# Kernel tuning notes

Hardware: AMD Instinct MI355X
Metric: run time of the kernel (lower is better)

The kernel has to match this reference:

```python
import jax, jax.numpy as jnp
import numpy as np

B, E = 256, 65536          # batch, embed_dim
S = 256                    # seq_len = sqrt(E)
D = E // S                 # per-token input dim = 256
HID = 512                  # hidden_dim
HD = HID // 2              # per-direction GRU hidden = 256
GH = 128                   # gcn_hidden_dim
K = 5                      # k_neighbors


def setup_inputs() -> dict:
    key = jax.random.key(0)
    ks = jax.random.split(key, 16)
    s = 0.02
    return {
        "C_masked": jax.random.normal(ks[0], (B, E), jnp.float32),
        "W_proj": jax.random.normal(ks[1], (HID, D), jnp.float32) * s,
        "b_proj": jnp.zeros((HID,), jnp.float32),
        "Wih_f": jax.random.normal(ks[2], (3 * HD, HID), jnp.float32) * s,
        "Whh_f": jax.random.normal(ks[3], (3 * HD, HD), jnp.float32) * s,
        "bih_f": jnp.zeros((3 * HD,), jnp.float32),
        "bhh_f": jnp.zeros((3 * HD,), jnp.float32),
        "Wih_b": jax.random.normal(ks[4], (3 * HD, HID), jnp.float32) * s,
        "Whh_b": jax.random.normal(ks[5], (3 * HD, HD), jnp.float32) * s,
        "bih_b": jnp.zeros((3 * HD,), jnp.float32),
        "bhh_b": jnp.zeros((3 * HD,), jnp.float32),
        "W_gcn1": jax.random.normal(ks[6], (HID, GH), jnp.float32) * 0.01,
        "W_gcn2": jax.random.normal(ks[7], (GH, HID), jnp.float32) * 0.01,
    }


def _gru_dir(x, Wih, Whh, bih, bhh, reverse):
    # x: (B, S, IN) -> (B, S, HD). PyTorch GRU cell equations.
    gi = jnp.einsum('bsd,hd->bsh', x, Wih) + bih          # (B,S,3HD)
    gi = jnp.swapaxes(gi, 0, 1)                            # (S,B,3HD)
    h0 = jnp.zeros((x.shape[0], HD), x.dtype)

    def step(h, gi_t):
        gh = h @ Whh.T + bhh
        i_r, i_z, i_n = jnp.split(gi_t, 3, axis=-1)
        h_r, h_z, h_n = jnp.split(gh, 3, axis=-1)
        r = jax.nn.sigmoid(i_r + h_r)
        z = jax.nn.sigmoid(i_z + h_z)
        n = jnp.tanh(i_n + r * h_n)
        h_new = (1.0 - z) * n + z * h
        return h_new, h_new

    _, ys = jax.lax.scan(step, h0, gi, reverse=reverse)    # (S,B,HD), index-aligned
    return jnp.swapaxes(ys, 0, 1)


def reference(C_masked, W_proj, b_proj,
              Wih_f, Whh_f, bih_f, bhh_f,
              Wih_b, Whh_b, bih_b, bhh_b,
              W_gcn1, W_gcn2):
    b, e = C_masked.shape
    s = int(np.sqrt(e))
    d = e // s
    C_seq = C_masked.reshape(b, s, d)
    C_proj = jnp.einsum('bsd,hd->bsh', C_seq, W_proj) + b_proj   # (B,S,HID)

    # BiGRU (eval mode; dropout inactive)
    h_f = _gru_dir(C_proj, Wih_f, Whh_f, bih_f, bhh_f, reverse=False)
    h_b = _gru_dir(C_proj, Wih_b, Whh_b, bih_b, bhh_b, reverse=True)
    H = jnp.concatenate([h_f, h_b], axis=-1)                     # (B,S,HID)

    # KNN graph: cosine sim -> topk -> scatter 1.0 -> add self loops
    Hn = H / jnp.maximum(jnp.linalg.norm(H, axis=-1, keepdims=True), 1e-12)
    sim = jnp.einsum('bnd,bmd->bnm', Hn, Hn)                     # (B,S,S)
    topk_idx = jax.lax.top_k(sim, K)[1]                          # (B,S,K)
    bi = jnp.arange(b)[:, None, None]
    ni = jnp.arange(s)[None, :, None]
    A = jnp.zeros((b, s, s), H.dtype).at[bi, ni, topk_idx].set(1.0)
    A = A + jnp.eye(s, dtype=H.dtype)[None]

    # D^{-1/2} A D^{-1/2}
    deg = A.sum(axis=-1) + 1e-8
    dinv = deg ** -0.5
    A_norm = dinv[:, :, None] * A * dinv[:, None, :]

    # 2-layer GCN (dropout inactive in eval)
    Z1 = jax.nn.relu(jnp.einsum('bnm,bmh->bnh', A_norm, H @ W_gcn1))
    Z = jnp.einsum('bnm,bmh->bnh', A_norm, Z1 @ W_gcn2)
    return Z
```

## Files before the change

kernel.cpp:

```cpp
#include <hip/hip_runtime.h>
#include <hip/hip_fp16.h>
#include <cstdint>
#include <cmath>

typedef _Float16 f16x8 __attribute__((ext_vector_type(8)));
typedef float f32x4 __attribute__((ext_vector_type(4)));

#define MFMA16(A, B, C) __builtin_amdgcn_mfma_f32_16x16x32_f16(A, B, C, 0, 0, 0)
#define LO_SCALE 2048.0f
#define LO_INV   4.8828125e-4f

#define GBM 128
#define GBN 128
#define GBK 16

template<bool TRANSB>
__global__ __launch_bounds__(256)
void gemm_f32(int M, int N, int K,
              const float* __restrict__ A, long long sA,
              const float* __restrict__ B, long long sB,
              float* __restrict__ Cc, long long sC,
              const float* __restrict__ bias,
              const float* __restrict__ rsA,
              const float* __restrict__ rsB)
{
    const int z = blockIdx.z;
    A  += (size_t)z * (size_t)sA;
    B  += (size_t)z * (size_t)sB;
    Cc += (size_t)z * (size_t)sC;

    const int bm = blockIdx.y * GBM;
    const int bn = blockIdx.x * GBN;
    const int tid = threadIdx.x;
    const int tx = tid & 15;
    const int ty = tid >> 4;

    __shared__ float As[GBK][GBM + 4];
    __shared__ float Bs[GBK][GBN + 4];

    float acc[8][8];
#pragma unroll
    for (int i = 0; i < 8; ++i)
#pragma unroll
        for (int j = 0; j < 8; ++j) acc[i][j] = 0.0f;

    const int lr = tid >> 2;
    const int lk = (tid & 3) << 2;
    const int kb_n = tid >> 5;
    const int nb_n = (tid & 31) << 2;

    float sa0 = 1.f, sa1 = 1.f, sb0 = 1.f, sb1 = 1.f;
    if (rsA) {
        sa0 = rsA[(size_t)z * M + bm + lr];
        sa1 = rsA[(size_t)z * M + bm + lr + 64];
    }
    if (TRANSB && rsB) {
        sb0 = rsB[(size_t)z * N + bn + lr];
        sb1 = rsB[(size_t)z * N + bn + lr + 64];
    }

    float4 pa0, pa1, pb0, pb1;

    auto gload = [&](int kt) {
        const float* pA = A + (size_t)(bm + lr) * K + kt * GBK + lk;
        pa0 = *(const float4*)pA;
        pa1 = *(const float4*)(pA + (size_t)64 * K);
        if (TRANSB) {
            const float* pB = B + (size_t)(bn + lr) * K + kt * GBK + lk;
            pb0 = *(const float4*)pB;
            pb1 = *(const float4*)(pB + (size_t)64 * K);
        } else {
            const float* pB = B + (size_t)(kt * GBK + kb_n) * N + bn + nb_n;
            pb0 = *(const float4*)pB;
            pb1 = *(const float4*)(pB + (size_t)8 * N);
        }
    };
    auto sstore = [&]() {
        As[lk + 0][lr] = pa0.x * sa0; As[lk + 1][lr] = pa0.y * sa0;
        As[lk + 2][lr] = pa0.z * sa0; As[lk + 3][lr] = pa0.w * sa0;
        As[lk + 0][lr + 64] = pa1.x * sa1; As[lk + 1][lr + 64] = pa1.y * sa1;
        As[lk + 2][lr + 64] = pa1.z * sa1; As[lk + 3][lr + 64] = pa1.w * sa1;
        if (TRANSB) {
            Bs[lk + 0][lr] = pb0.x * sb0; Bs[lk + 1][lr] = pb0.y * sb0;
            Bs[lk + 2][lr] = pb0.z * sb0; Bs[lk + 3][lr] = pb0.w * sb0;
            Bs[lk + 0][lr + 64] = pb1.x * sb1; Bs[lk + 1][lr + 64] = pb1.y * sb1;
            Bs[lk + 2][lr + 64] = pb1.z * sb1; Bs[lk + 3][lr + 64] = pb1.w * sb1;
        } else {
            *(float4*)&Bs[kb_n][nb_n]     = pb0;
            *(float4*)&Bs[kb_n + 8][nb_n] = pb1;
        }
    };

    const int nkt = K / GBK;
    gload(0);
    sstore();
    __syncthreads();
    for (int kt = 0; kt < nkt; ++kt) {
        if (kt + 1 < nkt) gload(kt + 1);
#pragma unroll
        for (int k = 0; k < GBK; ++k) {
            float4 a0 = *(const float4*)&As[k][ty * 8];
            float4 a1 = *(const float4*)&As[k][ty * 8 + 4];
            float4 b0 = *(const float4*)&Bs[k][tx * 8];
            float4 b1 = *(const float4*)&Bs[k][tx * 8 + 4];
            float av[8] = {a0.x, a0.y, a0.z, a0.w, a1.x, a1.y, a1.z, a1.w};
            float bv[8] = {b0.x, b0.y, b0.z, b0.w, b1.x, b1.y, b1.z, b1.w};
#pragma unroll
            for (int i = 0; i < 8; ++i)
#pragma unroll
                for (int j = 0; j < 8; ++j)
                    acc[i][j] = fmaf(av[i], bv[j], acc[i][j]);
        }
        __syncthreads();
        if (kt + 1 < nkt) { sstore(); __syncthreads(); }
    }

    float bb[8];
#pragma unroll
    for (int j = 0; j < 8; ++j) bb[j] = bias ? bias[bn + tx * 8 + j] : 0.0f;
#pragma unroll
    for (int i = 0; i < 8; ++i) {
        const int row = bm + ty * 8 + i;
        float* cp = Cc + (size_t)row * N + bn + tx * 8;
        float4 o0 = make_float4(acc[i][0] + bb[0], acc[i][1] + bb[1],
                                acc[i][2] + bb[2], acc[i][3] + bb[3]);
        float4 o1 = make_float4(acc[i][4] + bb[4], acc[i][5] + bb[5],
                                acc[i][6] + bb[6], acc[i][7] + bb[7]);
        *(float4*)cp = o0;
        *(float4*)(cp + 4) = o1;
    }
}

__global__ void bias_combine(const float* __restrict__ Wih, const float* __restrict__ b_proj,
                             const float* __restrict__ bih, float* __restrict__ bcomb)
{
    const int j = blockIdx.x * blockDim.x + threadIdx.x;
    if (j >= 768) return;
    float s = bih[j];
    for (int k = 0; k < 512; ++k) s = fmaf(Wih[(size_t)j * 512 + k], b_proj[k], s);
    bcomb[j] = s;
}

__global__ __launch_bounds__(256)
void pack_w(const float* __restrict__ W, unsigned short* __restrict__ pack)
{
    const int idx = blockIdx.x * 256 + threadIdx.x;
    if (idx >= 768 * 256) return;
    const int n = idx >> 8;
    const int k = idx & 255;
    const float w = W[idx];
    const __half hi = __float2half(w);
    const __half lo = __float2half((w - __half2float(hi)) * LO_SCALE);
    const int nt = n >> 4;
    const int lane = ((k >> 3) & 3) * 16 + (n & 15);
    const int j = k & 7;
    const int kc = k >> 5;
    const size_t base = ((size_t)(nt * 8 + kc) * 2) * 512 + lane * 8 + j;
    pack[base]       = __half_as_ushort(hi);
    pack[base + 512] = __half_as_ushort(lo);
}

__global__ __launch_bounds__(256)
void pack_bk(const float* __restrict__ W, unsigned short* __restrict__ pack,
             int K, int N)
{
    const int idx = blockIdx.x * 256 + threadIdx.x;
    if (idx >= K * N) return;
    const int k = idx / N;
    const int n = idx - k * N;
    const float w = W[idx];
    const __half hi = __float2half(w);
    const __half lo = __float2half((w - __half2float(hi)) * LO_SCALE);
    const int nt = n >> 4;
    const int kc = k >> 5;
    const int lane = ((k >> 3) & 3) * 16 + (n & 15);
    const int j = k & 7;
    const int KC = K >> 5;
    const size_t base = ((size_t)(nt * KC + kc) * 2) * 512 + lane * 8 + j;
    pack[base]       = __half_as_ushort(hi);
    pack[base + 512] = __half_as_ushort(lo);
}

__global__ __launch_bounds__(512)
void gi_gemm_c(const float* __restrict__ Cm, const unsigned short* __restrict__ pack,
               const float* __restrict__ bcomb, float* __restrict__ gi, int t0)
{
    const int tid = threadIdx.x;
    const int w = tid >> 6, l = tid & 63;
    const int l15 = l & 15, l4 = l >> 4;
    const int bgrp = blockIdx.x >> 1;
    const int half = blockIdx.x & 1;
    const size_t m0 = (size_t)bgrp * 256 + t0 + half * 64;
    const size_t o0 = (size_t)bgrp * 128 + half * 64;

    __shared__ unsigned short alds[2][64 * 256];

    {
        const int row = tid >> 3;
        const int seg = (tid & 7) * 32;
        const float4* src = (const float4*)(Cm + (m0 + row) * 256 + seg);
        const int sw = (row & 7) << 3;
#pragma unroll
        for (int i = 0; i < 8; ++i) {
            float4 v = src[i];
            float vv[4] = {v.x, v.y, v.z, v.w};
#pragma unroll
            for (int e = 0; e < 4; ++e) {
                const float x = vv[e];
                const __half hi = __float2half(x);
                const __half lo = __float2half((x - __half2float(hi)) * LO_SCALE);
                const int ad = (row << 8) + ((seg + i * 4 + e) ^ sw);
                alds[0][ad] = __half_as_ushort(hi);
                alds[1][ad] = __half_as_ushort(lo);
            }
        }
    }
    __syncthreads();

    const int mt = w >> 1, nh = w & 1;
    f32x4 acc[24];
#pragma unroll
    for (int i = 0; i < 24; ++i) acc[i] = (f32x4){0.f, 0.f, 0.f, 0.f};

    const int ar = mt * 16 + l15;
    const int arow = ar << 8;
    const int asw = (ar & 7) << 3;

#pragma unroll
    for (int kc = 0; kc < 8; ++kc) {
        const int ad = arow + ((kc * 32 + l4 * 8) ^ asw);
        const f16x8 ahi = *(const f16x8*)&alds[0][ad];
        const f16x8 alo = *(const f16x8*)&alds[1][ad];
#pragma unroll
        for (int nt = 0; nt < 24; ++nt) {
            const int nt_lin = nh * 24 + nt;
            const uint4* bp = (const uint4*)(pack + ((size_t)(nt_lin * 8 + kc) * 2) * 512);
            uint4 bh4 = bp[l];
            uint4 bl4 = bp[64 + l];
            const f16x8 Bhi = *reinterpret_cast<const f16x8*>(&bh4);
            const f16x8 Blo = *reinterpret_cast<const f16x8*>(&bl4);
            acc[nt] = MFMA16(ahi, Bhi, acc[nt]);
            f32x4 t2 = (f32x4){0.f, 0.f, 0.f, 0.f};
            t2 = MFMA16(ahi, Blo, t2);
            t2 = MFMA16(alo, Bhi, t2);
#pragma unroll
            for (int r = 0; r < 4; ++r) acc[nt][r] = fmaf(LO_INV, t2[r], acc[nt][r]);
        }
    }

#pragma unroll
    for (int nt = 0; nt < 24; ++nt) {
        const int n = (nh * 24 + nt) * 16 + l15;
        const float bb = bcomb[n];
#pragma unroll
        for (int r = 0; r < 4; ++r) {
            const size_t om = o0 + mt * 16 + l4 * 4 + r;
            __builtin_nontemporal_store(acc[nt][r] + bb, &gi[om * 768 + n]);
        }
    }
}

__global__ __launch_bounds__(1024)
void gru_scan_v9(const float* __restrict__ gi_fc, const float* __restrict__ gi_bc,
                 const float* __restrict__ Whh_f, const float* __restrict__ Whh_b,
                 const float* __restrict__ bhh_f, const float* __restrict__ bhh_b,
                 float* __restrict__ H, float* __restrict__ hstate, int phase)
{
    const int bid = blockIdx.x;
    const int xcd = bid & 7;
    const int dir = xcd >> 2;
    const int grp = (bid >> 3) * 4 + (xcd & 3);
    const float* __restrict__ gi  = dir ? gi_bc : gi_fc;
    const float* __restrict__ Whh = dir ? Whh_b : Whh_f;
    const float* __restrict__ bhh = dir ? bhh_b : bhh_f;
    const int b0 = grp * 8;
    const int t0 = dir ? (128 - phase * 128) : (phase * 128);

    const int tid = threadIdx.x;
    const int j = tid >> 2;
    const int q = tid & 3;
    const int bA = q, bB = q + 4;

    __shared__ float hb[2][8][256];

    float hregA, hregB;
    if (phase == 0) { hregA = 0.f; hregB = 0.f; }
    else {
        hregA = hstate[((size_t)dir * 256 + b0 + bA) * 256 + j];
        hregB = hstate[((size_t)dir * 256 + b0 + bB) * 256 + j];
    }
    hb[0][bA][j] = hregA;
    hb[0][bB][j] = hregB;

    const float bh_r = bhh[j], bh_z = bhh[j + 256], bh_n = bhh[j + 512];
    const float* __restrict__ Wr = Whh + (size_t)j * 256 + q * 4;
    const float* __restrict__ Wz = Whh + (size_t)(j + 256) * 256 + q * 4;
    const float* __restrict__ Wn = Whh + (size_t)(j + 512) * 256 + q * 4;

    __syncthreads();

    int p = 0;
    for (int tau = 0; tau < 128; ++tau) {
        const int sc = dir ? (127 - tau) : tau;
        const int tt = t0 + sc;

        const float* gpA = gi + ((size_t)(b0 + bA) * 128 + sc) * 768 + j;
        const float* gpB = gi + ((size_t)(b0 + bB) * 128 + sc) * 768 + j;
        const float grA = __builtin_nontemporal_load(gpA);
        const float gzA = __builtin_nontemporal_load(gpA + 256);
        const float gnA = __builtin_nontemporal_load(gpA + 512);
        const float grB = __builtin_nontemporal_load(gpB);
        const float gzB = __builtin_nontemporal_load(gpB + 256);
        const float gnB = __builtin_nontemporal_load(gpB + 512);

        float ar[8], az[8], an[8];
#pragma unroll
        for (int b = 0; b < 8; ++b) { ar[b] = 0.f; az[b] = 0.f; an[b] = 0.f; }

        float4 wrP[3], wzP[3], wnP[3];
#pragma unroll
        for (int i = 0; i < 3; ++i) {
            wrP[i] = *(const float4*)(Wr + i * 16);
            wzP[i] = *(const float4*)(Wz + i * 16);
            wnP[i] = *(const float4*)(Wn + i * 16);
        }

#pragma unroll
        for (int u = 0; u < 16; ++u) {
            const int s3 = u % 3;
            const float4 wr = wrP[s3], wz = wzP[s3], wn = wnP[s3];
            if (u + 3 < 16) {
                wrP[s3] = *(const float4*)(Wr + (u + 3) * 16);
                wzP[s3] = *(const float4*)(Wz + (u + 3) * 16);
                wnP[s3] = *(const float4*)(Wn + (u + 3) * 16);
            }
            const int ha = u * 16 + q * 4;
#pragma unroll
            for (int b = 0; b < 8; ++b) {
                const float4 hv = *(const float4*)&hb[p][b][ha];
                ar[b] = fmaf(wr.x, hv.x, ar[b]); ar[b] = fmaf(wr.y, hv.y, ar[b]);
                ar[b] = fmaf(wr.z, hv.z, ar[b]); ar[b] = fmaf(wr.w, hv.w, ar[b]);
                az[b] = fmaf(wz.x, hv.x, az[b]); az[b] = fmaf(wz.y, hv.y, az[b]);
                az[b] = fmaf(wz.z, hv.z, az[b]); az[b] = fmaf(wz.w, hv.w, az[b]);
                an[b] = fmaf(wn.x, hv.x, an[b]); an[b] = fmaf(wn.y, hv.y, an[b]);
                an[b] = fmaf(wn.z, hv.z, an[b]); an[b] = fmaf(wn.w, hv.w, an[b]);
            }
        }

#pragma unroll
        for (int b = 0; b < 8; ++b) {
            ar[b] += __shfl_xor(ar[b], 1); ar[b] += __shfl_xor(ar[b], 2);
            az[b] += __shfl_xor(az[b], 1); az[b] += __shfl_xor(az[b], 2);
            an[b] += __shfl_xor(an[b], 1); an[b] += __shfl_xor(an[b], 2);
        }

        const float prA = (q == 0) ? ar[0] : (q == 1) ? ar[1] : (q == 2) ? ar[2] : ar[3];
        const float pzA = (q == 0) ? az[0] : (q == 1) ? az[1] : (q == 2) ? az[2] : az[3];
        const float pnA = (q == 0) ? an[0] : (q == 1) ? an[1] : (q == 2) ? an[2] : an[3];
        const float prB = (q == 0) ? ar[4] : (q == 1) ? ar[5] : (q == 2) ? ar[6] : ar[7];
        const float pzB = (q == 0) ? az[4] : (q == 1) ? az[5] : (q == 2) ? az[6] : az[7];
        const float pnB = (q == 0) ? an[4] : (q == 1) ? an[5] : (q == 2) ? an[6] : an[7];

        float rr = 1.0f / (1.0f + expf(-(grA + prA + bh_r)));
        float zz = 1.0f / (1.0f + expf(-(gzA + pzA + bh_z)));
        float nn = tanhf(gnA + rr * (pnA + bh_n));
        hregA = (1.0f - zz) * nn + zz * hregA;
        rr = 1.0f / (1.0f + expf(-(grB + prB + bh_r)));
        zz = 1.0f / (1.0f + expf(-(gzB + pzB + bh_z)));
        nn = tanhf(gnB + rr * (pnB + bh_n));
        hregB = (1.0f - zz) * nn + zz * hregB;

        hb[p ^ 1][bA][j] = hregA;
        hb[p ^ 1][bB][j] = hregB;
        __builtin_nontemporal_store(
            hregA, &H[((size_t)(b0 + bA) * 256 + tt) * 512 + dir * 256 + j]);
        __builtin_nontemporal_store(
            hregB, &H[((size_t)(b0 + bB) * 256 + tt) * 512 + dir * 256 + j]);
        __syncthreads();
        p ^= 1;
    }

    hstate[((size_t)dir * 256 + b0 + bA) * 256 + j] = hregA;
    hstate[((size_t)dir * 256 + b0 + bB) * 256 + j] = hregB;
}

__global__ __launch_bounds__(256)
void rownorm(const float* __restrict__ H, float* __restrict__ rinv)
{
    const int row  = blockIdx.x * 4 + (threadIdx.x >> 6);
    const int lane = threadIdx.x & 63;
    const float4* p = (const float4*)(H + (size_t)row * 512);
    float ss = 0.f;
    float4 v = p[lane];
    ss += v.x * v.x + v.y * v.y + v.z * v.z + v.w * v.w;
    v = p[lane + 64];
    ss += v.x * v.x + v.y * v.y + v.z * v.z + v.w * v.w;
#pragma unroll
    for (int off = 32; off >= 1; off >>= 1) ss += __shfl_xor(ss, off);
    if (lane == 0) rinv[row] = 1.0f / fmaxf(sqrtf(ss), 1e-12f);
}

__global__ __launch_bounds__(512)
void sim_mfma(const float* __restrict__ H, const float* __restrict__ rinv,
              float* __restrict__ sim)
{
    const int b = blockIdx.x;
    const int tid = threadIdx.x;
    const int w = tid >> 6, l = tid & 63;
    const int l15 = l & 15, l4 = l >> 4;

    __shared__ unsigned short st[2][256][40];

    f32x4 acc[2][16];
#pragma unroll
    for (int m = 0; m < 2; ++m)
#pragma unroll
        for (int n = 0; n < 16; ++n) acc[m][n] = (f32x4){0.f, 0.f, 0.f, 0.f};

    const int sr = tid >> 1;
    const int sh = (tid & 1) * 16;
    const float rv = rinv[b * 256 + sr];
    const float* hrow = H + ((size_t)b * 256 + sr) * 512;

    for (int kc = 0; kc < 16; ++kc) {
        if (kc) __syncthreads();
        {
            const float4* src = (const float4*)(hrow + kc * 32 + sh);
#pragma unroll
            for (int i = 0; i < 4; ++i) {
                float4 v = src[i];
                float vv[4] = {v.x, v.y, v.z, v.w};
                ushort4 h4, l4v;
                unsigned short* hp = (unsigned short*)&h4;
                unsigned short* lp = (unsigned short*)&l4v;
#pragma unroll
                for (int e = 0; e < 4; ++e) {
                    const float x = vv[e] * rv;
                    const __half hi = __float2half(x);
                    const __half lo = __float2half((x - __half2float(hi)) * LO_SCALE);
                    hp[e] = __half_as_ushort(hi);
                    lp[e] = __half_as_ushort(lo);
                }
                *(ushort4*)&st[0][sr][sh + i * 4] = h4;
                *(ushort4*)&st[1][sr][sh + i * 4] = l4v;
            }
        }
        __syncthreads();

        f16x8 ahi[2], alo[2];
#pragma unroll
        for (int m = 0; m < 2; ++m) {
            const int row = (w * 2 + m) * 16 + l15;
            ahi[m] = *(const f16x8*)&st[0][row][l4 * 8];
            alo[m] = *(const f16x8*)&st[1][row][l4 * 8];
        }
#pragma unroll
        for (int nt = 0; nt < 16; ++nt) {
            const int col = nt * 16 + l15;
            const f16x8 bhi = *(const f16x8*)&st[0][col][l4 * 8];
            const f16x8 blo = *(const f16x8*)&st[1][col][l4 * 8];
#pragma unroll
            for (int m = 0; m < 2; ++m) {
                acc[m][nt] = MFMA16(ahi[m], bhi, acc[m][nt]);
                f32x4 t2 = (f32x4){0.f, 0.f, 0.f, 0.f};
                t2 = MFMA16(ahi[m], blo, t2);
                t2 = MFMA16(alo[m], bhi, t2);
#pragma unroll
                for (int r = 0; r < 4; ++r)
                    acc[m][nt][r] = fmaf(LO_INV, t2[r], acc[m][nt][r]);
            }
        }
    }

#pragma unroll
    for (int m = 0; m < 2; ++m) {
        const int row0 = (w * 2 + m) * 16 + l4 * 4;
#pragma unroll
        for (int nt = 0; nt < 16; ++nt)
#pragma unroll
            for (int r = 0; r < 4; ++r)
                sim[((size_t)b * 256 + row0 + r) * 256 + nt * 16 + l15] = acc[m][nt][r];
    }
}

template<int KDIM, int NDIM, int NT_PER>
__global__ __launch_bounds__(512)
void gcn_mm(const float* __restrict__ X, const unsigned short* __restrict__ pack,
            float* __restrict__ Y)
{
    const int tid = threadIdx.x;
    const int w = tid >> 6, l = tid & 63;
    const int l15 = l & 15, l4 = l >> 4;
    const int m0 = blockIdx.x * 64;
    constexpr int KC = KDIM / 32;

    __shared__ unsigned short a[2][64 * KDIM];

    {
        const int row = tid >> 3;
        const int seg = (tid & 7) * (KDIM / 8);
        const float4* src = (const float4*)(X + (size_t)(m0 + row) * KDIM + seg);
        const int sw = (row & 7) << 3;
#pragma unroll
        for (int i = 0; i < KDIM / 32; ++i) {
            float4 v = src[i];
            float vv[4] = {v.x, v.y, v.z, v.w};
#pragma unroll
            for (int e = 0; e < 4; ++e) {
                const float x = vv[e];
                const __half hi = __float2half(x);
                const __half lo = __float2half((x - __half2float(hi)) * LO_SCALE);
                const int ad = row * KDIM + ((seg + i * 4 + e) ^ sw);
                a[0][ad] = __half_as_ushort(hi);
                a[1][ad] = __half_as_ushort(lo);
            }
        }
    }
    __syncthreads();

    const int mt = w >> 1, nh = w & 1;
    f32x4 acc[NT_PER];
#pragma unroll
    for (int i = 0; i < NT_PER; ++i) acc[i] = (f32x4){0.f, 0.f, 0.f, 0.f};

    const int arow = mt * 16 + l15;
    const int abase = arow * KDIM;
    const int asw = (arow & 7) << 3;

#pragma unroll
    for (int kc = 0; kc < KC; ++kc) {
        const int ad = abase + ((kc * 32 + l4 * 8) ^ asw);
        const f16x8 ahi = *(const f16x8*)&a[0][ad];
        const f16x8 alo = *(const f16x8*)&a[1][ad];
#pragma unroll
        for (int ntl = 0; ntl < NT_PER; ++ntl) {
            const int nt = nh * NT_PER + ntl;
            const uint4* bp = (const uint4*)(pack + ((size_t)(nt * KC + kc) * 2) * 512);
            uint4 bh4 = bp[l];
            uint4 bl4 = bp[64 + l];
            const f16x8 Bhi = *reinterpret_cast<const f16x8*>(&bh4);
            const f16x8 Blo = *reinterpret_cast<const f16x8*>(&bl4);
            acc[ntl] = MFMA16(ahi, Bhi, acc[ntl]);
            f32x4 t2 = (f32x4){0.f, 0.f, 0.f, 0.f};
            t2 = MFMA16(ahi, Blo, t2);
            t2 = MFMA16(alo, Bhi, t2);
#pragma unroll
            for (int r = 0; r < 4; ++r) acc[ntl][r] = fmaf(LO_INV, t2[r], acc[ntl][r]);
        }
    }

#pragma unroll
    for (int ntl = 0; ntl < NT_PER; ++ntl) {
        const int n = (nh * NT_PER + ntl) * 16 + l15;
#pragma unroll
        for (int r = 0; r < 4; ++r) {
            const int m = m0 + mt * 16 + l4 * 4 + r;
            Y[(size_t)m * NDIM + n] = acc[ntl][r];
        }
    }
}

__global__ __launch_bounds__(256)
void topk5(const float* __restrict__ sim, int* __restrict__ idx)
{
    const int row = blockIdx.x * 256 + threadIdx.x;
    const float* p = sim + (size_t)row * 256;
    float bv0 = -1e30f, bv1 = -1e30f, bv2 = -1e30f, bv3 = -1e30f, bv4 = -1e30f;
    int   bi0 = 0, bi1 = 0, bi2 = 0, bi3 = 0, bi4 = 0;
    for (int m4 = 0; m4 < 64; ++m4) {
        float4 v4 = *(const float4*)(p + m4 * 4);
        float vv[4] = {v4.x, v4.y, v4.z, v4.w};
#pragma unroll
        for (int c = 0; c < 4; ++c) {
            float v = vv[c];
            int   m = m4 * 4 + c;
            if (v > bv0) {
                if (v > bv1) {
                    bv0 = bv1; bi0 = bi1;
                    if (v > bv2) {
                        bv1 = bv2; bi1 = bi2;
                        if (v > bv3) {
                            bv2 = bv3; bi2 = bi3;
                            if (v > bv4) { bv3 = bv4; bi3 = bi4; bv4 = v; bi4 = m; }
                            else         { bv3 = v;  bi3 = m; }
                        } else { bv2 = v; bi2 = m; }
                    } else { bv1 = v; bi1 = m; }
                } else { bv0 = v; bi0 = m; }
            }
        }
    }
    int* o = idx + (size_t)row * 5;
    o[0] = bi0; o[1] = bi1; o[2] = bi2; o[3] = bi3; o[4] = bi4;
}

template<bool RELU, int DIM>
__global__ __launch_bounds__(128)
void gcn_agg(const float* __restrict__ X, const int* __restrict__ idxs,
             float* __restrict__ outp, float cnorm)
{
    const int row = blockIdx.x;
    const int bbase = row & ~255;
    const int* id = idxs + (size_t)row * 5;
    const int i0 = bbase + id[0];
    const int i1 = bbase + id[1];
    const int i2 = bbase + id[2];
    const int i3 = bbase + id[3];
    const int i4 = bbase + id[4];
    const int t = threadIdx.x;
    if (DIM == 512) {
        const float4* Xp = (const float4*)X;
        float4 a = Xp[(size_t)row * 128 + t];
        float4 v;
        v = Xp[(size_t)i0 * 128 + t]; a.x += v.x; a.y += v.y; a.z += v.z; a.w += v.w;
        v = Xp[(size_t)i1 * 128 + t]; a.x += v.x; a.y += v.y; a.z += v.z; a.w += v.w;
        v = Xp[(size_t)i2 * 128 + t]; a.x += v.x; a.y += v.y; a.z += v.z; a.w += v.w;
        v = Xp[(size_t)i3 * 128 + t]; a.x += v.x; a.y += v.y; a.z += v.z; a.w += v.w;
        v = Xp[(size_t)i4 * 128 + t]; a.x += v.x; a.y += v.y; a.z += v.z; a.w += v.w;
        a.x *= cnorm; a.y *= cnorm; a.z *= cnorm; a.w *= cnorm;
        if (RELU) {
            a.x = fmaxf(a.x, 0.f); a.y = fmaxf(a.y, 0.f);
            a.z = fmaxf(a.z, 0.f); a.w = fmaxf(a.w, 0.f);
        }
        ((float4*)outp)[(size_t)row * 128 + t] = a;
    } else {
        float a = X[(size_t)row * 128 + t];
        a += X[(size_t)i0 * 128 + t];
        a += X[(size_t)i1 * 128 + t];
        a += X[(size_t)i2 * 128 + t];
        a += X[(size_t)i3 * 128 + t];
        a += X[(size_t)i4 * 128 + t];
        a *= cnorm;
        if (RELU) a = fmaxf(a, 0.f);
        outp[(size_t)row * 128 + t] = a;
    }
}

extern "C" void kernel_launch(void* const* d_in, const int* in_sizes, int n_in,
                              void* d_out, int out_size, void* d_ws, size_t ws_size,
                              hipStream_t stream)
{
    (void)in_sizes; (void)n_in; (void)out_size; (void)ws_size;

    const float* C_masked = (const float*)d_in[0];
    const float* W_proj   = (const float*)d_in[1];
    const float* b_proj   = (const float*)d_in[2];
    const float* Wih_f    = (const float*)d_in[3];
    const float* Whh_f    = (const float*)d_in[4];
    const float* bih_f    = (const float*)d_in[5];
    const float* bhh_f    = (const float*)d_in[6];
    const float* Wih_b    = (const float*)d_in[7];
    const float* Whh_b    = (const float*)d_in[8];
    const float* bih_b    = (const float*)d_in[9];
    const float* bhh_b    = (const float*)d_in[10];
    const float* W_gcn1   = (const float*)d_in[11];
    const float* W_gcn2   = (const float*)d_in[12];
    float* out = (float*)d_out;

    char* ws = (char*)d_ws;
    size_t o = 0;
    auto take = [&](size_t bytes) {
        size_t r = o;
        o = (o + bytes + 255) & ~(size_t)255;
        return r;
    };
    const size_t WCOMB_B = (size_t)768 * 256 * 4;
    const size_t PACK_B  = (size_t)48 * 8 * 2 * 512 * 2;
    const size_t PACKG_B = (size_t)262144;
    const size_t o_wcf  = take(WCOMB_B);
    const size_t o_wcb  = take(WCOMB_B);
    const size_t o_bcf  = take(768 * 4);
    const size_t o_bcb  = take(768 * 4);
    const size_t o_rinv = take((size_t)65536 * 4);
    const size_t o_topk = take((size_t)65536 * 5 * 4);
    const size_t o_pwf  = take(PACK_B);
    const size_t o_pwb  = take(PACK_B);
    const size_t o_pg1  = take(PACKG_B);
    const size_t o_pg2  = take(PACKG_B);
    const size_t o_hst  = take((size_t)512 * 256 * 4);
    const size_t regionA = o;

    const size_t GIC_BYTES = (size_t)256 * 128 * 768 * 4;

    float* wcomb_f = (float*)(ws + o_wcf);
    float* wcomb_b = (float*)(ws + o_wcb);
    float* bcomb_f = (float*)(ws + o_bcf);
    float* bcomb_b = (float*)(ws + o_bcb);
    float* rinv    = (float*)(ws + o_rinv);
    int*   topk    = (int*)(ws + o_topk);
    unsigned short* packWf = (unsigned short*)(ws + o_pwf);
    unsigned short* packWb = (unsigned short*)(ws + o_pwb);
    unsigned short* packG1 = (unsigned short*)(ws + o_pg1);
    unsigned short* packG2 = (unsigned short*)(ws + o_pg2);
    float* hstate = (float*)(ws + o_hst);

    float* gi_fc = (float*)(ws + regionA);
    float* gi_bc = (float*)(ws + regionA + GIC_BYTES);
    float* Hbuf  = (float*)(ws + regionA + 2 * GIC_BYTES);

    float* sim  = (float*)(ws + regionA);
    float* XW1  = (float*)(ws + regionA + 67108864);
    float* Z1   = (float*)(ws + regionA + 100663296);
    float* Z1W2 = (float*)(ws + regionA);

    const dim3 blk(256);

    gemm_f32<false><<<dim3(2, 6, 1), blk, 0, stream>>>(
        768, 256, 512, Wih_f, 0, W_proj, 0, wcomb_f, 0, nullptr, nullptr, nullptr);
    gemm_f32<false><<<dim3(2, 6, 1), blk, 0, stream>>>(
        768, 256, 512, Wih_b, 0, W_proj, 0, wcomb_b, 0, nullptr, nullptr, nullptr);
    bias_combine<<<3, 256, 0, stream>>>(Wih_f, b_proj, bih_f, bcomb_f);
    bias_combine<<<3, 256, 0, stream>>>(Wih_b, b_proj, bih_b, bcomb_b);
    pack_w<<<768, 256, 0, stream>>>(wcomb_f, packWf);
    pack_w<<<768, 256, 0, stream>>>(wcomb_b, packWb);
    pack_bk<<<256, 256, 0, stream>>>(W_gcn1, packG1, 512, 128);
    pack_bk<<<256, 256, 0, stream>>>(W_gcn2, packG2, 128, 512);

    gi_gemm_c<<<512, 512, 0, stream>>>(C_masked, packWf, bcomb_f, gi_fc, 0);
    gi_gemm_c<<<512, 512, 0, stream>>>(C_masked, packWb, bcomb_b, gi_bc, 128);
    gru_scan_v9<<<64, 1024, 0, stream>>>(gi_fc, gi_bc, Whh_f, Whh_b,
                                         bhh_f, bhh_b, Hbuf, hstate, 0);
    gi_gemm_c<<<512, 512, 0, stream>>>(C_masked, packWf, bcomb_f, gi_fc, 128);
    gi_gemm_c<<<512, 512, 0, stream>>>(C_masked, packWb, bcomb_b, gi_bc, 0);
    gru_scan_v9<<<64, 1024, 0, stream>>>(gi_fc, gi_bc, Whh_f, Whh_b,
                                         bhh_f, bhh_b, Hbuf, hstate, 1);

    rownorm<<<16384, blk, 0, stream>>>(Hbuf, rinv);
    sim_mfma<<<256, 512, 0, stream>>>(Hbuf, rinv, sim);
    topk5<<<256, blk, 0, stream>>>(sim, topk);

    const float cnorm = (float)(1.0 / (6.0 + 1e-8));
    gcn_mm<512, 128, 4><<<1024, 512, 0, stream>>>(Hbuf, packG1, XW1);
    gcn_agg<true, 128><<<65536, 128, 0, stream>>>(XW1, topk, Z1, cnorm);
    gcn_mm<128, 512, 16><<<1024, 512, 0, stream>>>(Z1, packG2, Z1W2);
    gcn_agg<false, 512><<<65536, 128, 0, stream>>>(Z1W2, topk, out, cnorm);
}
```

Baseline: 6.763 ms.

## Repack GRU recurrent weights for coalesced loads and prefetch next-step gate inputs

Adds a pack kernel that rearranges Whh into a thread-contiguous float4 layout, so each thread's weight loads in the recurrent scan are fully coalesced instead of strided across rows. The scan now double-buffers weight chunks in registers and software-pipelines the gi loads one timestep ahead. It also sets a launch_bounds occupancy hint. The cost is two extra small pack launches, extra workspace, and higher register pressure in the scan.

```diff
diff --git a/kernel.cpp b/kernel.cpp
--- a/kernel.cpp
+++ b/kernel.cpp
@@ -181,6 +181,21 @@
     pack[base + 512] = __half_as_ushort(lo);
 }
 
+__global__ __launch_bounds__(256)
+void pack_wsc(const float* __restrict__ W, float* __restrict__ wpk)
+{
+    const int idx = blockIdx.x * 256 + threadIdx.x;
+    if (idx >= 768 * 256) return;
+    const int row = idx >> 8;
+    const int k   = idx & 255;
+    const int g = row >> 8;
+    const int j = row & 255;
+    const int u = k >> 4;
+    const int q = (k >> 2) & 3;
+    const int e = k & 3;
+    wpk[(((size_t)(u * 3 + g) * 1024) + (j << 2) + q) * 4 + e] = W[idx];
+}
+
 __global__ __launch_bounds__(512)
 void gi_gemm_c(const float* __restrict__ Cm, const unsigned short* __restrict__ pack,
                const float* __restrict__ bcomb, float* __restrict__ gi, int t0)
@@ -260,18 +275,18 @@
     }
 }
 
-__global__ __launch_bounds__(1024)
-void gru_scan_v9(const float* __restrict__ gi_fc, const float* __restrict__ gi_bc,
-                 const float* __restrict__ Whh_f, const float* __restrict__ Whh_b,
-                 const float* __restrict__ bhh_f, const float* __restrict__ bhh_b,
-                 float* __restrict__ H, float* __restrict__ hstate, int phase)
+__global__ __launch_bounds__(1024, 4)
+void gru_scan_v12(const float* __restrict__ gi_fc, const float* __restrict__ gi_bc,
+                  const float* __restrict__ wpk_f, const float* __restrict__ wpk_b,
+                  const float* __restrict__ bhh_f, const float* __restrict__ bhh_b,
+                  float* __restrict__ H, float* __restrict__ hstate, int phase)
 {
     const int bid = blockIdx.x;
     const int xcd = bid & 7;
     const int dir = xcd >> 2;
     const int grp = (bid >> 3) * 4 + (xcd & 3);
     const float* __restrict__ gi  = dir ? gi_bc : gi_fc;
-    const float* __restrict__ Whh = dir ? Whh_b : Whh_f;
+    const float4* __restrict__ Wp = (const float4*)(dir ? wpk_b : wpk_f);
     const float* __restrict__ bhh = dir ? bhh_b : bhh_f;
     const int b0 = grp * 8;
     const int t0 = dir ? (128 - phase * 128) : (phase * 128);
@@ -293,57 +308,84 @@
     hb[0][bB][j] = hregB;
 
     const float bh_r = bhh[j], bh_z = bhh[j + 256], bh_n = bhh[j + 512];
-    const float* __restrict__ Wr = Whh + (size_t)j * 256 + q * 4;
-    const float* __restrict__ Wz = Whh + (size_t)(j + 256) * 256 + q * 4;
-    const float* __restrict__ Wn = Whh + (size_t)(j + 512) * 256 + q * 4;
 
     __syncthreads();
+
+    const int sc00 = dir ? 127 : 0;
+    const float* gA0 = gi + ((size_t)(b0 + bA) * 128 + sc00) * 768 + j;
+    const float* gB0 = gi + ((size_t)(b0 + bB) * 128 + sc00) * 768 + j;
+    float grA = __builtin_nontemporal_load(gA0);
+    float gzA = __builtin_nontemporal_load(gA0 + 256);
+    float gnA = __builtin_nontemporal_load(gA0 + 512);
+    float grB = __builtin_nontemporal_load(gB0);
+    float gzB = __builtin_nontemporal_load(gB0 + 256);
+    float gnB = __builtin_nontemporal_load(gB0 + 512);
 
     int p = 0;
     for (int tau = 0; tau < 128; ++tau) {
         const int sc = dir ? (127 - tau) : tau;
         const int tt = t0 + sc;
 
-        const float* gpA = gi + ((size_t)(b0 + bA) * 128 + sc) * 768 + j;
-        const float* gpB = gi + ((size_t)(b0 + bB) * 128 + sc) * 768 + j;
-        const float grA = __builtin_nontemporal_load(gpA);
-        const float gzA = __builtin_nontemporal_load(gpA + 256);
-        const float gnA = __builtin_nontemporal_load(gpA + 512);
-        const float grB = __builtin_nontemporal_load(gpB);
-        const float gzB = __builtin_nontemporal_load(gpB + 256);
-        const float gnB = __builtin_nontemporal_load(gpB + 512);
+        const float g_rA = grA, g_zA = gzA, g_nA = gnA;
+        const float g_rB = grB, g_zB = gzB, g_nB = gnB;
+        if (tau < 127) {
+            const int scn = dir ? (126 - tau) : (tau + 1);
+            const float* gA = gi + ((size_t)(b0 + bA) * 128 + scn) * 768 + j;
+            const float* gB = gi + ((size_t)(b0 + bB) * 128 + scn) * 768 + j;
+            grA = __builtin_nontemporal_load(gA);
+            gzA = __builtin_nontemporal_load(gA + 256);
+            gnA = __builtin_nontemporal_load(gA + 512);
+            grB = __builtin_nontemporal_load(gB);
+            gzB = __builtin_nontemporal_load(gB + 256);
+            gnB = __builtin_nontemporal_load(gB + 512);
+        }
 
         float ar[8], az[8], an[8];
 #pragma unroll
         for (int b = 0; b < 8; ++b) { ar[b] = 0.f; az[b] = 0.f; an[b] = 0.f; }
 
-        float4 wrP[3], wzP[3], wnP[3];
-#pragma unroll
-        for (int i = 0; i < 3; ++i) {
-            wrP[i] = *(const float4*)(Wr + i * 16);
-            wzP[i] = *(const float4*)(Wz + i * 16);
-            wnP[i] = *(const float4*)(Wn + i * 16);
-        }
-
-#pragma unroll
-        for (int u = 0; u < 16; ++u) {
-            const int s3 = u % 3;
-            const float4 wr = wrP[s3], wz = wzP[s3], wn = wnP[s3];
-            if (u + 3 < 16) {
-                wrP[s3] = *(const float4*)(Wr + (u + 3) * 16);
-                wzP[s3] = *(const float4*)(Wz + (u + 3) * 16);
-                wnP[s3] = *(const float4*)(Wn + (u + 3) * 16);
+        float4 wb0[6], wb1[6];
+#pragma unroll
+        for (int s = 0; s < 2; ++s) {
+            wb0[s * 3 + 0] = Wp[((s) * 3 + 0) * 1024 + tid];
+            wb0[s * 3 + 1] = Wp[((s) * 3 + 1) * 1024 + tid];
+            wb0[s * 3 + 2] = Wp[((s) * 3 + 2) * 1024 + tid];
+        }
+
+#pragma unroll
+        for (int c = 0; c < 8; ++c) {
+            if (c < 7) {
+#pragma unroll
+                for (int s = 0; s < 2; ++s) {
+                    const int uu = (c + 1) * 2 + s;
+                    if (c & 1) {
+                        wb0[s * 3 + 0] = Wp[(uu * 3 + 0) * 1024 + tid];
+                        wb0[s * 3 + 1] = Wp[(uu * 3 + 1) * 1024 + tid];
+                        wb0[s * 3 + 2] = Wp[(uu * 3 + 2) * 1024 + tid];
+                    } else {
+                        wb1[s * 3 + 0] = Wp[(uu * 3 + 0) * 1024 + tid];
+                        wb1[s * 3 + 1] = Wp[(uu * 3 + 1) * 1024 + tid];
+                        wb1[s * 3 + 2] = Wp[(uu * 3 + 2) * 1024 + tid];
+                    }
+                }
             }
-            const int ha = u * 16 + q * 4;
-#pragma unroll
-            for (int b = 0; b < 8; ++b) {
-                const float4 hv = *(const float4*)&hb[p][b][ha];
-                ar[b] = fmaf(wr.x, hv.x, ar[b]); ar[b] = fmaf(wr.y, hv.y, ar[b]);
-                ar[b] = fmaf(wr.z, hv.z, ar[b]); ar[b] = fmaf(wr.w, hv.w, ar[b]);
-                az[b] = fmaf(wz.x, hv.x, az[b]); az[b] = fmaf(wz.y, hv.y, az[b]);
-                az[b] = fmaf(wz.z, hv.z, az[b]); az[b] = fmaf(wz.w, hv.w, az[b]);
-                an[b] = fmaf(wn.x, hv.x, an[b]); an[b] = fmaf(wn.y, hv.y, an[b]);
-                an[b] = fmaf(wn.z, hv.z, an[b]); an[b] = fmaf(wn.w, hv.w, an[b]);
+#pragma unroll
+            for (int s = 0; s < 2; ++s) {
+                const int u = c * 2 + s;
+                const float4 wr = (c & 1) ? wb1[s * 3 + 0] : wb0[s * 3 + 0];
+                const float4 wz = (c & 1) ? wb1[s * 3 + 1] : wb0[s * 3 + 1];
+                const float4 wn = (c & 1) ? wb1[s * 3 + 2] : wb0[s * 3 + 2];
+                const int ha = u * 16 + q * 4;
+#pragma unroll
+                for (int b = 0; b < 8; ++b) {
+                    const float4 hv = *(const float4*)&hb[p][b][ha];
+                    ar[b] = fmaf(wr.x, hv.x, ar[b]); ar[b] = fmaf(wr.y, hv.y, ar[b]);
+                    ar[b] = fmaf(wr.z, hv.z, ar[b]); ar[b] = fmaf(wr.w, hv.w, ar[b]);
+                    az[b] = fmaf(wz.x, hv.x, az[b]); az[b] = fmaf(wz.y, hv.y, az[b]);
+                    az[b] = fmaf(wz.z, hv.z, az[b]); az[b] = fmaf(wz.w, hv.w, az[b]);
+                    an[b] = fmaf(wn.x, hv.x, an[b]); an[b] = fmaf(wn.y, hv.y, an[b]);
+                    an[b] = fmaf(wn.z, hv.z, an[b]); an[b] = fmaf(wn.w, hv.w, an[b]);
+                }
             }
         }
 
@@ -361,13 +403,13 @@
         const float pzB = (q == 0) ? az[4] : (q == 1) ? az[5] : (q == 2) ? az[6] : az[7];
         const float pnB = (q == 0) ? an[4] : (q == 1) ? an[5] : (q == 2) ? an[6] : an[7];
 
-        float rr = 1.0f / (1.0f + expf(-(grA + prA + bh_r)));
-        float zz = 1.0f / (1.0f + expf(-(gzA + pzA + bh_z)));
-        float nn = tanhf(gnA + rr * (pnA + bh_n));
+        float rr = 1.0f / (1.0f + expf(-(g_rA + prA + bh_r)));
+        float zz = 1.0f / (1.0f + expf(-(g_zA + pzA + bh_z)));
+        float nn = tanhf(g_nA + rr * (pnA + bh_n));
         hregA = (1.0f - zz) * nn + zz * hregA;
-        rr = 1.0f / (1.0f + expf(-(grB + prB + bh_r)));
-        zz = 1.0f / (1.0f + expf(-(gzB + pzB + bh_z)));
-        nn = tanhf(gnB + rr * (pnB + bh_n));
+        rr = 1.0f / (1.0f + expf(-(g_rB + prB + bh_r)));
+        zz = 1.0f / (1.0f + expf(-(g_zB + pzB + bh_z)));
+        nn = tanhf(g_nB + rr * (pnB + bh_n));
         hregB = (1.0f - zz) * nn + zz * hregB;
 
         hb[p ^ 1][bA][j] = hregA;
@@ -674,6 +716,8 @@
     const size_t o_topk = take((size_t)65536 * 5 * 4);
     const size_t o_pwf  = take(PACK_B);
     const size_t o_pwb  = take(PACK_B);
+    const size_t o_wsf  = take(WCOMB_B);
+    const size_t o_wsb  = take(WCOMB_B);
     const size_t o_pg1  = take(PACKG_B);
     const size_t o_pg2  = take(PACKG_B);
     const size_t o_hst  = take((size_t)512 * 256 * 4);
@@ -689,6 +733,8 @@
     int*   topk    = (int*)(ws + o_topk);
     unsigned short* packWf = (unsigned short*)(ws + o_pwf);
     unsigned short* packWb = (unsigned short*)(ws + o_pwb);
+    float* wpkF = (float*)(ws + o_wsf);
+    float* wpkB = (float*)(ws + o_wsb);
     unsigned short* packG1 = (unsigned short*)(ws + o_pg1);
     unsigned short* packG2 = (unsigned short*)(ws + o_pg2);
     float* hstate = (float*)(ws + o_hst);
@@ -712,17 +758,19 @@
     bias_combine<<<3, 256, 0, stream>>>(Wih_b, b_proj, bih_b, bcomb_b);
     pack_w<<<768, 256, 0, stream>>>(wcomb_f, packWf);
     pack_w<<<768, 256, 0, stream>>>(wcomb_b, packWb);
+    pack_wsc<<<768, 256, 0, stream>>>(Whh_f, wpkF);
+    pack_wsc<<<768, 256, 0, stream>>>(Whh_b, wpkB);
     pack_bk<<<256, 256, 0, stream>>>(W_gcn1, packG1, 512, 128);
     pack_bk<<<256, 256, 0, stream>>>(W_gcn2, packG2, 128, 512);
 
     gi_gemm_c<<<512, 512, 0, stream>>>(C_masked, packWf, bcomb_f, gi_fc, 0);
     gi_gemm_c<<<512, 512, 0, stream>>>(C_masked, packWb, bcomb_b, gi_bc, 128);
-    gru_scan_v9<<<64, 1024, 0, stream>>>(gi_fc, gi_bc, Whh_f, Whh_b,
-                                         bhh_f, bhh_b, Hbuf, hstate, 0);
+    gru_scan_v12<<<64, 1024, 0, stream>>>(gi_fc, gi_bc, wpkF, wpkB,
+                                          bhh_f, bhh_b, Hbuf, hstate, 0);
     gi_gemm_c<<<512, 512, 0, stream>>>(C_masked, packWf, bcomb_f, gi_fc, 128);
     gi_gemm_c<<<512, 512, 0, stream>>>(C_masked, packWb, bcomb_b, gi_bc, 0);
-    gru_scan_v9<<<64, 1024, 0, stream>>>(gi_fc, gi_bc, Whh_f, Whh_b,
-                                         bhh_f, bhh_b, Hbuf, hstate, 1);
+    gru_scan_v12<<<64, 1024, 0, stream>>>(gi_fc, gi_bc, wpkF, wpkB,
+                                          bhh_f, bhh_b, Hbuf, hstate, 1);
 
     rownorm<<<16384, blk, 0, stream>>>(Hbuf, rinv);
     sim_mfma<<<256, 512, 0, stream>>>(Hbuf, rinv, sim);
```

Result: slower. 7.553 ms (+11.7%).
